# Kernel tuning notes

Hardware: AMD Instinct MI355X
Metric: run time of the kernel (lower is better)

Reference implementation:

```python
import jax, jax.numpy as jnp
import numpy as np

N_NODES = 50000
N_EDGES = 500000
H = 128          # h_dim
HEADS = 3
B = 512          # histories with non-zero length
L = 10           # seq_len (all histories full length)
N_RELS = 200
NEG_SLOPE = 0.2  # DGL GATConv default negative_slope


def setup_inputs() -> dict:
    key = jax.random.key(0)
    ks = jax.random.split(key, 18)
    p = lambda i, shape: jax.random.normal(ks[i], shape, jnp.float32) * 0.05
    return {
        "node_feat": jax.random.normal(ks[0], (N_NODES, H), jnp.float32),
        "W1": p(1, (H, HEADS * H)),
        "attn_l1": p(2, (HEADS, H)),
        "attn_r1": p(3, (HEADS, H)),
        "b1": p(4, (HEADS * H,)),
        "W2": p(5, (H, HEADS * H)),
        "attn_l2": p(6, (HEADS, H)),
        "attn_r2": p(7, (HEADS, H)),
        "b2": p(8, (HEADS * H,)),
        "ent_embeds": jax.random.normal(ks[9], (N_NODES, H), jnp.float32),
        "rel_embeds": jax.random.normal(ks[10], (N_RELS, H), jnp.float32),
        "global_emb_list": jax.random.normal(ks[11], (B * L, H), jnp.float32),
        "s_hist_t": jax.random.uniform(ks[12], (B, L), jnp.float32),
        "edge_src": jax.random.randint(ks[13], (N_EDGES,), 0, N_NODES),
        "edge_dst": jax.random.randint(ks[14], (N_EDGES,), 0, N_NODES),
        "node_ids_graph": jax.random.randint(ks[15], (B * L,), 0, N_NODES),
        "s_tem": jax.random.randint(ks[16], (B,), 0, N_NODES),
        "r_tem": jax.random.randint(ks[17], (B,), 0, N_RELS),
    }


def gat_conv(x, W, attn_l, attn_r, bias, src, dst):
    """DGL-style GATConv (allow_zero_in_degree=True, eval mode)."""
    n = x.shape[0]
    feat = (x @ W).reshape(n, HEADS, H)                    # [N, heads, H]
    el = jnp.einsum('nhd,hd->nh', feat, attn_l)            # [N, heads]
    er = jnp.einsum('nhd,hd->nh', feat, attn_r)
    e = jax.nn.leaky_relu(el[src] + er[dst], NEG_SLOPE)    # [E, heads]
    # edge softmax over incoming edges of each dst node
    emax = jax.ops.segment_max(e, dst, num_segments=n)
    ex = jnp.exp(e - emax[dst])
    denom = jax.ops.segment_sum(ex, dst, num_segments=n)
    alpha = ex / denom[dst]                                # [E, heads]
    msg = alpha[:, :, None] * feat[src]                    # [E, heads, H]
    rst = jax.ops.segment_sum(msg, dst, num_segments=n)    # [N, heads, H]
    return rst + bias.reshape(1, HEADS, H)


def reference(node_feat, W1, attn_l1, attn_r1, b1, W2, attn_l2, attn_r2, b2,
              ent_embeds, rel_embeds, global_emb_list, s_hist_t,
              edge_src, edge_dst, node_ids_graph, s_tem, r_tem):
    h = gat_conv(node_feat, W1, attn_l1, attn_r1, b1, edge_src, edge_dst).mean(axis=1)
    h = gat_conv(h, W2, attn_l2, attn_r2, b2, edge_src, edge_dst).mean(axis=1)
    embeds = h[node_ids_graph].reshape(B, L, H)            # gathered history node embeds
    ent = jnp.broadcast_to(ent_embeds[s_tem][:, None, :], (B, L, H))
    rel = jnp.broadcast_to(rel_embeds[r_tem][:, None, :], (B, L, H))
    glob = global_emb_list.reshape(B, L, H)
    seq = jnp.concatenate([embeds, ent, rel, glob], axis=-1)   # [B, L, 4H]
    seq_r = jnp.concatenate([embeds, ent, glob], axis=-1)      # [B, L, 3H]
    return seq, seq_r, s_hist_t
```

## Files before the change

kernel.cpp:

```cpp
#include <hip/hip_runtime.h>
#include <hip/hip_bf16.h>

#define N_NODES 50000
#define N_EDGES 500000
#define HDIM 128
#define HEADS 3
#define BB 512
#define LL 10
#define NEG_SLOPE 0.2f

typedef __hip_bfloat16 bf16;
typedef unsigned char fp8t;
typedef __bf16 v8bf __attribute__((ext_vector_type(8)));
typedef float f32x4 __attribute__((ext_vector_type(4)));


__global__ void k_zero2(int* a, int na, int* b, int nb){
  int i = blockIdx.x*256 + threadIdx.x;
  if(i < na) a[i] = 0;
  if(i < nb) b[i] = 0;
}

__global__ void k_hist(const int* __restrict__ dst, int* __restrict__ cnt, int E){
  int e = blockIdx.x*256 + threadIdx.x;
  if(e < E) atomicAdd(&cnt[dst[e]], 1);
}


#define SCAN_TILE 2048
#define SCAN_NB ((N_NODES + SCAN_TILE - 1)/SCAN_TILE)

__global__ __launch_bounds__(256) void k_scan_part(const int* __restrict__ cnt,
                                                   int* __restrict__ bsum){
  int b = blockIdx.x, tid = threadIdx.x;
  int i0 = b*SCAN_TILE + tid*8;
  int s = 0;
  #pragma unroll
  for(int j = 0; j < 8; ++j){ int i = i0 + j; s += (i < N_NODES) ? cnt[i] : 0; }
  for(int m = 32; m; m >>= 1) s += __shfl_xor(s, m);
  __shared__ int ws[4];
  if((tid & 63) == 0) ws[tid >> 6] = s;
  __syncthreads();
  if(tid == 0) bsum[b] = ws[0] + ws[1] + ws[2] + ws[3];
}

__global__ __launch_bounds__(64) void k_scan_top(int* __restrict__ bsum, int nb){
  int tid = threadIdx.x;
  int v = (tid < nb) ? bsum[tid] : 0;
  for(int s = 1; s < 64; s <<= 1){
    int t = __shfl_up(v, s);
    if(tid >= s) v += t;
  }
  if(tid < nb) bsum[tid] = v;
}

__global__ __launch_bounds__(256) void k_scan_write(int* __restrict__ cnt,
                                                    const int* __restrict__ bsum,
                                                    int* __restrict__ offs){
  int b = blockIdx.x, tid = threadIdx.x;
  int lane = tid & 63, wv = tid >> 6;
  int i0 = b*SCAN_TILE + tid*8;
  int v[8]; int s = 0;
  #pragma unroll
  for(int j = 0; j < 8; ++j){
    int i = i0 + j;
    v[j] = (i < N_NODES) ? cnt[i] : 0;
    s += v[j];
  }
  #pragma unroll
  for(int j = 0; j < 8; ++j){ int i = i0 + j; if(i < N_NODES) cnt[i] = 0; }
  int incl = s;
  for(int sh = 1; sh < 64; sh <<= 1){
    int t = __shfl_up(incl, sh);
    if(lane >= sh) incl += t;
  }
  __shared__ int wtot[4];
  if(lane == 63) wtot[wv] = incl;
  __syncthreads();
  int woff = 0;
  for(int w = 0; w < wv; ++w) woff += wtot[w];
  int excl = woff + incl - s;
  int run = ((b > 0) ? bsum[b-1] : 0) + excl;
  #pragma unroll
  for(int j = 0; j < 8; ++j){
    int i = i0 + j;
    run += v[j];
    if(i < N_NODES) offs[i+1] = run;
  }
  if(b == 0 && tid == 0) offs[0] = 0;
}

__global__ void k_scatter(const int* __restrict__ src, const int* __restrict__ dst,
                          const int* __restrict__ offs, int* __restrict__ cur,
                          int* __restrict__ csr, int E){
  int e = blockIdx.x*256 + threadIdx.x;
  if(e < E){
    int d = dst[e];
    int p = offs[d] + atomicAdd(&cur[d], 1);
    if(p >= 0 && p < E) csr[p] = src[e];
  }
}


__global__ __launch_bounds__(64) void k_mark(const int* __restrict__ nid,
                                             const int* __restrict__ offs,
                                             const int* __restrict__ csr,
                                             unsigned char* __restrict__ mark){
  unsigned n = (unsigned)nid[blockIdx.x];
  if(n >= N_NODES) return;
  if(threadIdx.x == 0) mark[n] = 1;
  int o0 = offs[n], o1 = offs[n+1];
  for(int j = o0 + (int)threadIdx.x; j < o1; j += 64){
    unsigned s = (unsigned)csr[j];
    if(s < N_NODES) mark[s] = 1;
  }
}


__global__ void k_wt(const float* __restrict__ W, bf16* __restrict__ Wt){
  int i = blockIdx.x*256 + threadIdx.x;
  if(i < HEADS*HDIM*HDIM){
    int n = i >> 7, k = i & 127;
    Wt[i] = __float2bfloat16(W[k*(HEADS*HDIM) + n]);
  }
}


template<int AF32>
__global__ __launch_bounds__(256) void k_gemm(const void* __restrict__ Av,
                                              const bf16* __restrict__ Wt,
                                              const float* __restrict__ al,
                                              const float* __restrict__ ar,
                                              fp8t* __restrict__ feat8,
                                              float* __restrict__ el4,
                                              float* __restrict__ er4, int M){
  int tid  = threadIdx.x;
  int wave = tid >> 6, lane = tid & 63;
  int wr = wave >> 1, wc = wave & 1;
  int row0 = blockIdx.x*64 + wr*32;
  int col0 = blockIdx.y*128 + wc*64;
  int l15 = lane & 15, lhi = lane >> 4;

  f32x4 acc[2][4] = {};
  for(int kk = 0; kk < 4; ++kk){
    int kb = kk*32 + lhi*8;
    v8bf a[2], b[4];
    for(int mi = 0; mi < 2; ++mi){
      int r = row0 + mi*16 + l15;
      if(r >= M) r = M - 1;
      if constexpr(AF32){
        const float* ap = (const float*)Av + (size_t)r*HDIM + kb;
        f32x4 lo = *reinterpret_cast<const f32x4*>(ap);
        f32x4 hi = *reinterpret_cast<const f32x4*>(ap + 4);
        #pragma unroll
        for(int j = 0; j < 4; ++j){ a[mi][j] = (__bf16)lo[j]; a[mi][4+j] = (__bf16)hi[j]; }
      } else {
        a[mi] = *reinterpret_cast<const v8bf*>((const bf16*)Av + (size_t)r*HDIM + kb);
      }
    }
    for(int ni = 0; ni < 4; ++ni){
      int c = col0 + ni*16 + l15;
      b[ni] = *reinterpret_cast<const v8bf*>(Wt + (size_t)c*HDIM + kb);
    }
    for(int mi = 0; mi < 2; ++mi)
      for(int ni = 0; ni < 4; ++ni)
        acc[mi][ni] = __builtin_amdgcn_mfma_f32_16x16x32_bf16(a[mi], b[ni], acc[mi][ni], 0, 0, 0);
  }

  const float* alh = al + blockIdx.y*HDIM;
  const float* arh = ar + blockIdx.y*HDIM;
  float alv[4], arv[4];
  #pragma unroll
  for(int ni = 0; ni < 4; ++ni){
    int d = wc*64 + ni*16 + l15;
    alv[ni] = alh[d]; arv[ni] = arh[d];
  }
  __shared__ float red[2][64][2];
  __shared__ int4 tile4[512];
  fp8t* tile8 = (fp8t*)tile4;

  #pragma unroll
  for(int mi = 0; mi < 2; ++mi){
    #pragma unroll
    for(int j = 0; j < 4; ++j){
      float pe = 0.f, pr = 0.f;
      #pragma unroll
      for(int ni = 0; ni < 4; ++ni){
        pe += acc[mi][ni][j]*alv[ni];
        pr += acc[mi][ni][j]*arv[ni];
      }
      for(int k = 8; k; k >>= 1){ pe += __shfl_xor(pe, k); pr += __shfl_xor(pr, k); }
      int row_l = wr*32 + mi*16 + lhi*4 + j;
      if(l15 == 0){ red[wc][row_l][0] = pe; red[wc][row_l][1] = pr; }
    }
  }
  #pragma unroll
  for(int mi = 0; mi < 2; ++mi)
    #pragma unroll
    for(int j = 0; j < 4; ++j){
      int row_l = wr*32 + mi*16 + lhi*4 + j;
      #pragma unroll
      for(int ni = 0; ni < 4; ++ni){
        float x = acc[mi][ni][j];
        unsigned bb = (unsigned)__builtin_amdgcn_cvt_pk_fp8_f32(x, x, 0, false) & 0xFFu;
        tile8[row_l*128 + wc*64 + ni*16 + l15] = (fp8t)bb;
      }
    }
  __syncthreads();

  if(tid < 64){
    int r = blockIdx.x*64 + tid;
    if(r < M){
      el4[(size_t)r*4 + blockIdx.y] = red[0][tid][0] + red[1][tid][0];
      er4[(size_t)r*4 + blockIdx.y] = red[0][tid][1] + red[1][tid][1];
    }
  }
  #pragma unroll
  for(int pass = 0; pass < 2; ++pass){
    int off = pass*4096 + tid*16;
    int row_l = off >> 7, col = off & 127;
    int r = blockIdx.x*64 + row_l;
    if(r < M)
      *reinterpret_cast<int4*>(feat8 + (size_t)r*(HEADS*HDIM) + blockIdx.y*HDIM + col) =
          tile4[off >> 4];
  }
}


__device__ __forceinline__ float lrelu(float x){ return x > 0.f ? x : NEG_SLOPE*x; }
__device__ __forceinline__ float cvt8(fp8t b){
  return __builtin_amdgcn_cvt_f32_fp8((int)b, 0);
}

#define AGG_CHUNK 128

template<int USE_LIST, int OUT_F32, int USE_MARK>
__global__ __launch_bounds__(128) void k_agg(const fp8t* __restrict__ feat8,
                                             const float* __restrict__ el4,
                                             const float* __restrict__ er4,
                                             const float* __restrict__ bias,
                                             const int* __restrict__ offs,
                                             const int* __restrict__ csr,
                                             const int* __restrict__ list,
                                             const unsigned char* __restrict__ mark,
                                             void* __restrict__ hout){
  int bid = blockIdx.x;
  int n = USE_LIST ? list[bid] : bid;
  if(USE_MARK){ if(!mark[n]) return; }
  int tid = threadIdx.x, lane = tid & 63, wv = tid >> 6;
  __shared__ float s_m[2][3], s_s[2][3];
  __shared__ float s_alpha[AGG_CHUNK][4];
  __shared__ int   s_src[AGG_CHUNK];
  __shared__ float s_facc[HEADS*HDIM];
  int o0 = offs[n];
  int deg = offs[n+1] - o0;
  if(deg < 0 || deg > N_EDGES) deg = 0;
  float4 erv = *reinterpret_cast<const float4*>(er4 + (size_t)n*4);

  if(deg <= AGG_CHUNK){
    float x0 = -1e30f, x1 = -1e30f, x2 = -1e30f; int s = 0;
    if(tid < deg){
      unsigned su = (unsigned)csr[o0 + tid];
      if(su >= N_NODES) su = 0;
      s = (int)su;
      float4 elv = *reinterpret_cast<const float4*>(el4 + (size_t)s*4);
      x0 = lrelu(elv.x + erv.x);
      x1 = lrelu(elv.y + erv.y);
      x2 = lrelu(elv.z + erv.z);
    }
    float m0 = x0, m1 = x1, m2 = x2;
    for(int k = 32; k; k >>= 1){
      m0 = fmaxf(m0, __shfl_xor(m0, k));
      m1 = fmaxf(m1, __shfl_xor(m1, k));
      m2 = fmaxf(m2, __shfl_xor(m2, k));
    }
    if(lane == 0){ s_m[wv][0] = m0; s_m[wv][1] = m1; s_m[wv][2] = m2; }
    __syncthreads();
    m0 = fmaxf(s_m[0][0], s_m[1][0]);
    m1 = fmaxf(s_m[0][1], s_m[1][1]);
    m2 = fmaxf(s_m[0][2], s_m[1][2]);
    float e0 = (tid < deg) ? __expf(x0 - m0) : 0.f;
    float e1 = (tid < deg) ? __expf(x1 - m1) : 0.f;
    float e2 = (tid < deg) ? __expf(x2 - m2) : 0.f;
    float t0 = e0, t1 = e1, t2 = e2;
    for(int k = 32; k; k >>= 1){
      t0 += __shfl_xor(t0, k); t1 += __shfl_xor(t1, k); t2 += __shfl_xor(t2, k);
    }
    if(lane == 0){ s_s[wv][0] = t0; s_s[wv][1] = t1; s_s[wv][2] = t2; }
    if(tid < deg){
      s_src[tid] = s;
      s_alpha[tid][0] = e0; s_alpha[tid][1] = e1; s_alpha[tid][2] = e2;
    }
    __syncthreads();
    if(tid < 96){
      int head = tid >> 5;
      float S = s_s[0][head] + s_s[1][head];
      float ih = (S > 0.f) ? 1.f/S : 0.f;
      float a0 = 0.f, a1 = 0.f, a2 = 0.f, a3 = 0.f;
      for(int i = 0; i < deg; ++i){
        unsigned u = *reinterpret_cast<const unsigned*>(
            feat8 + (size_t)s_src[i]*(HEADS*HDIM) + tid*4);
        float al = s_alpha[i][head];
        a0 += al*__builtin_amdgcn_cvt_f32_fp8((int)u, 0);
        a1 += al*__builtin_amdgcn_cvt_f32_fp8((int)u, 1);
        a2 += al*__builtin_amdgcn_cvt_f32_fp8((int)u, 2);
        a3 += al*__builtin_amdgcn_cvt_f32_fp8((int)u, 3);
      }
      float4 w; w.x = a0*ih; w.y = a1*ih; w.z = a2*ih; w.w = a3*ih;
      *reinterpret_cast<float4*>(s_facc + tid*4) = w;
    }
    __syncthreads();
    float r = (s_facc[tid] + s_facc[HDIM + tid] + s_facc[2*HDIM + tid]
             + bias[tid] + bias[HDIM + tid] + bias[2*HDIM + tid])*(1.f/3.f);
    if(OUT_F32) ((float*)hout)[(size_t)bid*HDIM + tid] = r;
    else        ((bf16*)hout)[(size_t)bid*HDIM + tid] = __float2bfloat16(r);
    return;
  }

  float M0 = -1e30f, M1 = -1e30f, M2 = -1e30f;
  float S0 = 0.f, S1 = 0.f, S2 = 0.f;
  for(int base = 0; base < deg; base += AGG_CHUNK){
    int cn = min(AGG_CHUNK, deg - base);
    float x0 = -1e30f, x1 = -1e30f, x2 = -1e30f;
    if(tid < cn){
      unsigned su = (unsigned)csr[o0 + base + tid];
      if(su >= N_NODES) su = 0;
      float4 elv = *reinterpret_cast<const float4*>(el4 + (size_t)su*4);
      x0 = lrelu(elv.x + erv.x);
      x1 = lrelu(elv.y + erv.y);
      x2 = lrelu(elv.z + erv.z);
    }
    float m0 = x0, m1 = x1, m2 = x2;
    for(int k = 32; k; k >>= 1){
      m0 = fmaxf(m0, __shfl_xor(m0, k));
      m1 = fmaxf(m1, __shfl_xor(m1, k));
      m2 = fmaxf(m2, __shfl_xor(m2, k));
    }
    if(lane == 0){ s_m[wv][0] = m0; s_m[wv][1] = m1; s_m[wv][2] = m2; }
    __syncthreads();
    float nm0 = fmaxf(M0, fmaxf(s_m[0][0], s_m[1][0]));
    float nm1 = fmaxf(M1, fmaxf(s_m[0][1], s_m[1][1]));
    float nm2 = fmaxf(M2, fmaxf(s_m[0][2], s_m[1][2]));
    float e0 = (tid < cn) ? __expf(x0 - nm0) : 0.f;
    float e1 = (tid < cn) ? __expf(x1 - nm1) : 0.f;
    float e2 = (tid < cn) ? __expf(x2 - nm2) : 0.f;
    float t0 = e0, t1 = e1, t2 = e2;
    for(int k = 32; k; k >>= 1){
      t0 += __shfl_xor(t0, k); t1 += __shfl_xor(t1, k); t2 += __shfl_xor(t2, k);
    }
    if(lane == 0){ s_s[wv][0] = t0; s_s[wv][1] = t1; s_s[wv][2] = t2; }
    __syncthreads();
    S0 = S0*__expf(M0 - nm0) + s_s[0][0] + s_s[1][0];
    S1 = S1*__expf(M1 - nm1) + s_s[0][1] + s_s[1][1];
    S2 = S2*__expf(M2 - nm2) + s_s[0][2] + s_s[1][2];
    M0 = nm0; M1 = nm1; M2 = nm2;
  }
  float i0 = 1.f/S0, i1 = 1.f/S1, i2 = 1.f/S2;

  float a0 = 0.f, a1 = 0.f, a2 = 0.f;
  for(int base = 0; base < deg; base += AGG_CHUNK){
    int cn = min(AGG_CHUNK, deg - base);
    __syncthreads();
    if(tid < cn){
      unsigned su = (unsigned)csr[o0 + base + tid];
      if(su >= N_NODES) su = 0;
      float4 elv = *reinterpret_cast<const float4*>(el4 + (size_t)su*4);
      s_src[tid] = (int)su;
      s_alpha[tid][0] = __expf(lrelu(elv.x + erv.x) - M0)*i0;
      s_alpha[tid][1] = __expf(lrelu(elv.y + erv.y) - M1)*i1;
      s_alpha[tid][2] = __expf(lrelu(elv.z + erv.z) - M2)*i2;
    }
    __syncthreads();
    for(int i = 0; i < cn; ++i){
      const fp8t* fr = feat8 + (size_t)s_src[i]*(HEADS*HDIM);
      a0 += s_alpha[i][0]*cvt8(fr[tid]);
      a1 += s_alpha[i][1]*cvt8(fr[HDIM + tid]);
      a2 += s_alpha[i][2]*cvt8(fr[2*HDIM + tid]);
    }
  }
  float r = (a0 + a1 + a2 + bias[tid] + bias[HDIM+tid] + bias[2*HDIM+tid])*(1.f/3.f);
  if(OUT_F32) ((float*)hout)[(size_t)bid*HDIM + tid] = r;
  else        ((bf16*)hout)[(size_t)bid*HDIM + tid] = __float2bfloat16(r);
}


#define SEQ_SZ   (BB*LL*4*HDIM)
#define SEQR_OFF SEQ_SZ
#define SEQR_SZ  (BB*LL*3*HDIM)
#define SH_OFF   (SEQ_SZ + SEQR_SZ)

__global__ __launch_bounds__(128) void k_assemble(const float* __restrict__ h2s,
                                                  const float* __restrict__ ent_e,
                                                  const float* __restrict__ rel_e,
                                                  const float* __restrict__ glob,
                                                  const float* __restrict__ sht,
                                                  const int* __restrict__ s_tem,
                                                  const int* __restrict__ r_tem,
                                                  float* __restrict__ out){
  int p = blockIdx.x;
  int d = threadIdx.x;
  int b = p / LL;
  float emb = h2s[(size_t)p*HDIM + d];
  float ent = ent_e[(size_t)s_tem[b]*HDIM + d];
  float rel = rel_e[(size_t)r_tem[b]*HDIM + d];
  float gl  = glob[(size_t)p*HDIM + d];
  size_t so = (size_t)p*(4*HDIM);
  out[so + d] = emb; out[so + HDIM + d] = ent;
  out[so + 2*HDIM + d] = rel; out[so + 3*HDIM + d] = gl;
  size_t ro = SEQR_OFF + (size_t)p*(3*HDIM);
  out[ro + d] = emb; out[ro + HDIM + d] = ent; out[ro + 2*HDIM + d] = gl;
  if(d == 0) out[SH_OFF + p] = sht[p];
}


extern "C" void kernel_launch(void* const* d_in, const int* in_sizes, int n_in,
                              void* d_out, int out_size, void* d_ws, size_t ws_size,
                              hipStream_t stream){
  const float* node_feat = (const float*)d_in[0];
  const float* W1        = (const float*)d_in[1];
  const float* attn_l1   = (const float*)d_in[2];
  const float* attn_r1   = (const float*)d_in[3];
  const float* b1        = (const float*)d_in[4];
  const float* W2        = (const float*)d_in[5];
  const float* attn_l2   = (const float*)d_in[6];
  const float* attn_r2   = (const float*)d_in[7];
  const float* b2        = (const float*)d_in[8];
  const float* ent_emb   = (const float*)d_in[9];
  const float* rel_emb   = (const float*)d_in[10];
  const float* glob      = (const float*)d_in[11];
  const float* sht       = (const float*)d_in[12];
  const int*  e_src      = (const int*)d_in[13];
  const int*  e_dst      = (const int*)d_in[14];
  const int*  nid        = (const int*)d_in[15];
  const int*  s_tem      = (const int*)d_in[16];
  const int*  r_tem      = (const int*)d_in[17];
  float* out = (float*)d_out;

  char* ws = (char*)d_ws;
  size_t cur_off = 0;
  auto alloc = [&](size_t bytes)->char*{
    char* r = ws + cur_off;
    cur_off += (bytes + 255) & ~(size_t)255;
    return r;
  };
  fp8t*  feat8 = (fp8t*) alloc((size_t)N_NODES*HEADS*HDIM);
  bf16*  h1    = (bf16*) alloc((size_t)N_NODES*HDIM*2);
  float* h2s   = (float*)alloc((size_t)BB*LL*HDIM*4);
  float* el4   = (float*)alloc((size_t)N_NODES*4*4);
  float* er4   = (float*)alloc((size_t)N_NODES*4*4);
  bf16*  wt1   = (bf16*) alloc((size_t)HEADS*HDIM*HDIM*2);
  bf16*  wt2   = (bf16*) alloc((size_t)HEADS*HDIM*HDIM*2);
  int*   offs  = (int*)  alloc((size_t)(N_NODES+1)*4);
  int*   cnt   = (int*)  alloc((size_t)N_NODES*4);
  int*   bsum  = (int*)  alloc((size_t)SCAN_NB*4);
  unsigned char* mark = (unsigned char*)alloc((size_t)N_NODES);
  int*   csr   = (int*)  alloc((size_t)N_EDGES*4);

  k_zero2<<<(N_NODES+255)/256, 256, 0, stream>>>(cnt, N_NODES,
                                                 (int*)mark, (N_NODES+3)/4);
  k_hist<<<(N_EDGES+255)/256, 256, 0, stream>>>(e_dst, cnt, N_EDGES);
  k_scan_part<<<SCAN_NB, 256, 0, stream>>>(cnt, bsum);
  k_scan_top<<<1, 64, 0, stream>>>(bsum, SCAN_NB);
  k_scan_write<<<SCAN_NB, 256, 0, stream>>>(cnt, bsum, offs);
  k_scatter<<<(N_EDGES+255)/256, 256, 0, stream>>>(e_src, e_dst, offs, cnt, csr, N_EDGES);
  k_mark<<<BB*LL, 64, 0, stream>>>(nid, offs, csr, mark);

  k_wt<<<(HEADS*HDIM*HDIM+255)/256, 256, 0, stream>>>(W1, wt1);
  k_wt<<<(HEADS*HDIM*HDIM+255)/256, 256, 0, stream>>>(W2, wt2);

  dim3 ggrid((N_NODES + 63)/64, HEADS);

  k_gemm<1><<<ggrid, 256, 0, stream>>>((const void*)node_feat, wt1, attn_l1, attn_r1,
                                       feat8, el4, er4, N_NODES);
  k_agg<0,0,1><<<N_NODES, 128, 0, stream>>>(feat8, el4, er4, b1, offs, csr,
                                            nullptr, mark, (void*)h1);

  k_gemm<0><<<ggrid, 256, 0, stream>>>((const void*)h1, wt2, attn_l2, attn_r2,
                                       feat8, el4, er4, N_NODES);
  k_agg<1,1,0><<<BB*LL, 128, 0, stream>>>(feat8, el4, er4, b2, offs, csr,
                                          nid, nullptr, (void*)h2s);

  k_assemble<<<BB*LL, 128, 0, stream>>>(h2s, ent_emb, rel_emb, glob, sht,
                                        s_tem, r_tem, out);
}
```

Baseline: 212.8 us.

## Precompute softmax denominators in a separate pass and fuse assembly into aggregation

Adds a per-node kernel that sums the exponentiated attention logits and stores reciprocal denominators, without subtracting the per-node max. The aggregation kernel then computes normalized alphas directly, removing the in-block max and sum wave reductions and their barriers. The final output-assembly kernel is folded into the second aggregation, which drops the h2s intermediate buffer and one launch. The trade-off is an extra launch per layer, and skipping max subtraction risks exp overflow if logits grow large.

```diff
diff --git a/kernel.cpp b/kernel.cpp
--- a/kernel.cpp
+++ b/kernel.cpp
@@ -228,27 +228,70 @@
 
 
 __device__ __forceinline__ float lrelu(float x){ return x > 0.f ? x : NEG_SLOPE*x; }
-__device__ __forceinline__ float cvt8(fp8t b){
-  return __builtin_amdgcn_cvt_f32_fp8((int)b, 0);
-}
+
+template<int USE_LIST, int USE_MARK>
+__global__ __launch_bounds__(256) void k_denom(const float* __restrict__ el4,
+                                               const float* __restrict__ er4,
+                                               const int* __restrict__ offs,
+                                               const int* __restrict__ csr,
+                                               const int* __restrict__ list,
+                                               const unsigned char* __restrict__ mark,
+                                               float* __restrict__ inv4, int total){
+  int i = blockIdx.x*256 + threadIdx.x;
+  if(i >= total) return;
+  unsigned n = USE_LIST ? (unsigned)list[i] : (unsigned)i;
+  if(n >= N_NODES) return;
+  if(USE_MARK){ if(!mark[n]) return; }
+  int o0 = offs[n];
+  int deg = offs[n+1] - o0;
+  if(deg < 0 || deg > N_EDGES) deg = 0;
+  float4 erv = *reinterpret_cast<const float4*>(er4 + (size_t)n*4);
+  float S0 = 0.f, S1 = 0.f, S2 = 0.f;
+  for(int j = 0; j < deg; ++j){
+    unsigned s = (unsigned)csr[o0 + j];
+    if(s >= N_NODES) s = 0;
+    float4 elv = *reinterpret_cast<const float4*>(el4 + (size_t)s*4);
+    S0 += __expf(lrelu(elv.x + erv.x));
+    S1 += __expf(lrelu(elv.y + erv.y));
+    S2 += __expf(lrelu(elv.z + erv.z));
+  }
+  float4 iv;
+  iv.x = (S0 > 0.f) ? 1.f/S0 : 0.f;
+  iv.y = (S1 > 0.f) ? 1.f/S1 : 0.f;
+  iv.z = (S2 > 0.f) ? 1.f/S2 : 0.f;
+  iv.w = 0.f;
+  *reinterpret_cast<float4*>(inv4 + (size_t)n*4) = iv;
+}
+
 
 #define AGG_CHUNK 128
-
-template<int USE_LIST, int OUT_F32, int USE_MARK>
+#define SEQ_SZ   (BB*LL*4*HDIM)
+#define SEQR_OFF SEQ_SZ
+#define SEQR_SZ  (BB*LL*3*HDIM)
+#define SH_OFF   (SEQ_SZ + SEQR_SZ)
+
+template<int USE_LIST, int FUSED, int USE_MARK>
 __global__ __launch_bounds__(128) void k_agg(const fp8t* __restrict__ feat8,
                                              const float* __restrict__ el4,
                                              const float* __restrict__ er4,
+                                             const float* __restrict__ inv4,
                                              const float* __restrict__ bias,
                                              const int* __restrict__ offs,
                                              const int* __restrict__ csr,
                                              const int* __restrict__ list,
                                              const unsigned char* __restrict__ mark,
-                                             void* __restrict__ hout){
+                                             bf16* __restrict__ h1,
+                                             const float* __restrict__ ent_e,
+                                             const float* __restrict__ rel_e,
+                                             const float* __restrict__ glob,
+                                             const float* __restrict__ sht,
+                                             const int* __restrict__ s_tem,
+                                             const int* __restrict__ r_tem,
+                                             float* __restrict__ out){
   int bid = blockIdx.x;
   int n = USE_LIST ? list[bid] : bid;
   if(USE_MARK){ if(!mark[n]) return; }
-  int tid = threadIdx.x, lane = tid & 63, wv = tid >> 6;
-  __shared__ float s_m[2][3], s_s[2][3];
+  int tid = threadIdx.x;
   __shared__ float s_alpha[AGG_CHUNK][4];
   __shared__ int   s_src[AGG_CHUNK];
   __shared__ float s_facc[HEADS*HDIM];
@@ -256,48 +299,25 @@
   int deg = offs[n+1] - o0;
   if(deg < 0 || deg > N_EDGES) deg = 0;
   float4 erv = *reinterpret_cast<const float4*>(er4 + (size_t)n*4);
-
-  if(deg <= AGG_CHUNK){
-    float x0 = -1e30f, x1 = -1e30f, x2 = -1e30f; int s = 0;
-    if(tid < deg){
-      unsigned su = (unsigned)csr[o0 + tid];
+  float4 iv  = *reinterpret_cast<const float4*>(inv4 + (size_t)n*4);
+
+  float a0 = 0.f, a1 = 0.f, a2 = 0.f, a3 = 0.f;
+  int head = tid >> 5;
+  for(int base = 0; base < deg; base += AGG_CHUNK){
+    int cn = min(AGG_CHUNK, deg - base);
+    if(base) __syncthreads();
+    if(tid < cn){
+      unsigned su = (unsigned)csr[o0 + base + tid];
       if(su >= N_NODES) su = 0;
-      s = (int)su;
-      float4 elv = *reinterpret_cast<const float4*>(el4 + (size_t)s*4);
-      x0 = lrelu(elv.x + erv.x);
-      x1 = lrelu(elv.y + erv.y);
-      x2 = lrelu(elv.z + erv.z);
-    }
-    float m0 = x0, m1 = x1, m2 = x2;
-    for(int k = 32; k; k >>= 1){
-      m0 = fmaxf(m0, __shfl_xor(m0, k));
-      m1 = fmaxf(m1, __shfl_xor(m1, k));
-      m2 = fmaxf(m2, __shfl_xor(m2, k));
-    }
-    if(lane == 0){ s_m[wv][0] = m0; s_m[wv][1] = m1; s_m[wv][2] = m2; }
-    __syncthreads();
-    m0 = fmaxf(s_m[0][0], s_m[1][0]);
-    m1 = fmaxf(s_m[0][1], s_m[1][1]);
-    m2 = fmaxf(s_m[0][2], s_m[1][2]);
-    float e0 = (tid < deg) ? __expf(x0 - m0) : 0.f;
-    float e1 = (tid < deg) ? __expf(x1 - m1) : 0.f;
-    float e2 = (tid < deg) ? __expf(x2 - m2) : 0.f;
-    float t0 = e0, t1 = e1, t2 = e2;
-    for(int k = 32; k; k >>= 1){
-      t0 += __shfl_xor(t0, k); t1 += __shfl_xor(t1, k); t2 += __shfl_xor(t2, k);
-    }
-    if(lane == 0){ s_s[wv][0] = t0; s_s[wv][1] = t1; s_s[wv][2] = t2; }
-    if(tid < deg){
-      s_src[tid] = s;
-      s_alpha[tid][0] = e0; s_alpha[tid][1] = e1; s_alpha[tid][2] = e2;
+      float4 elv = *reinterpret_cast<const float4*>(el4 + (size_t)su*4);
+      s_src[tid] = (int)su;
+      s_alpha[tid][0] = __expf(lrelu(elv.x + erv.x))*iv.x;
+      s_alpha[tid][1] = __expf(lrelu(elv.y + erv.y))*iv.y;
+      s_alpha[tid][2] = __expf(lrelu(elv.z + erv.z))*iv.z;
     }
     __syncthreads();
     if(tid < 96){
-      int head = tid >> 5;
-      float S = s_s[0][head] + s_s[1][head];
-      float ih = (S > 0.f) ? 1.f/S : 0.f;
-      float a0 = 0.f, a1 = 0.f, a2 = 0.f, a3 = 0.f;
-      for(int i = 0; i < deg; ++i){
+      for(int i = 0; i < cn; ++i){
         unsigned u = *reinterpret_cast<const unsigned*>(
             feat8 + (size_t)s_src[i]*(HEADS*HDIM) + tid*4);
         float al = s_alpha[i][head];
@@ -306,110 +326,29 @@
         a2 += al*__builtin_amdgcn_cvt_f32_fp8((int)u, 2);
         a3 += al*__builtin_amdgcn_cvt_f32_fp8((int)u, 3);
       }
-      float4 w; w.x = a0*ih; w.y = a1*ih; w.z = a2*ih; w.w = a3*ih;
-      *reinterpret_cast<float4*>(s_facc + tid*4) = w;
-    }
-    __syncthreads();
-    float r = (s_facc[tid] + s_facc[HDIM + tid] + s_facc[2*HDIM + tid]
-             + bias[tid] + bias[HDIM + tid] + bias[2*HDIM + tid])*(1.f/3.f);
-    if(OUT_F32) ((float*)hout)[(size_t)bid*HDIM + tid] = r;
-    else        ((bf16*)hout)[(size_t)bid*HDIM + tid] = __float2bfloat16(r);
-    return;
-  }
-
-  float M0 = -1e30f, M1 = -1e30f, M2 = -1e30f;
-  float S0 = 0.f, S1 = 0.f, S2 = 0.f;
-  for(int base = 0; base < deg; base += AGG_CHUNK){
-    int cn = min(AGG_CHUNK, deg - base);
-    float x0 = -1e30f, x1 = -1e30f, x2 = -1e30f;
-    if(tid < cn){
-      unsigned su = (unsigned)csr[o0 + base + tid];
-      if(su >= N_NODES) su = 0;
-      float4 elv = *reinterpret_cast<const float4*>(el4 + (size_t)su*4);
-      x0 = lrelu(elv.x + erv.x);
-      x1 = lrelu(elv.y + erv.y);
-      x2 = lrelu(elv.z + erv.z);
-    }
-    float m0 = x0, m1 = x1, m2 = x2;
-    for(int k = 32; k; k >>= 1){
-      m0 = fmaxf(m0, __shfl_xor(m0, k));
-      m1 = fmaxf(m1, __shfl_xor(m1, k));
-      m2 = fmaxf(m2, __shfl_xor(m2, k));
-    }
-    if(lane == 0){ s_m[wv][0] = m0; s_m[wv][1] = m1; s_m[wv][2] = m2; }
-    __syncthreads();
-    float nm0 = fmaxf(M0, fmaxf(s_m[0][0], s_m[1][0]));
-    float nm1 = fmaxf(M1, fmaxf(s_m[0][1], s_m[1][1]));
-    float nm2 = fmaxf(M2, fmaxf(s_m[0][2], s_m[1][2]));
-    float e0 = (tid < cn) ? __expf(x0 - nm0) : 0.f;
-    float e1 = (tid < cn) ? __expf(x1 - nm1) : 0.f;
-    float e2 = (tid < cn) ? __expf(x2 - nm2) : 0.f;
-    float t0 = e0, t1 = e1, t2 = e2;
-    for(int k = 32; k; k >>= 1){
-      t0 += __shfl_xor(t0, k); t1 += __shfl_xor(t1, k); t2 += __shfl_xor(t2, k);
-    }
-    if(lane == 0){ s_s[wv][0] = t0; s_s[wv][1] = t1; s_s[wv][2] = t2; }
-    __syncthreads();
-    S0 = S0*__expf(M0 - nm0) + s_s[0][0] + s_s[1][0];
-    S1 = S1*__expf(M1 - nm1) + s_s[0][1] + s_s[1][1];
-    S2 = S2*__expf(M2 - nm2) + s_s[0][2] + s_s[1][2];
-    M0 = nm0; M1 = nm1; M2 = nm2;
-  }
-  float i0 = 1.f/S0, i1 = 1.f/S1, i2 = 1.f/S2;
-
-  float a0 = 0.f, a1 = 0.f, a2 = 0.f;
-  for(int base = 0; base < deg; base += AGG_CHUNK){
-    int cn = min(AGG_CHUNK, deg - base);
-    __syncthreads();
-    if(tid < cn){
-      unsigned su = (unsigned)csr[o0 + base + tid];
-      if(su >= N_NODES) su = 0;
-      float4 elv = *reinterpret_cast<const float4*>(el4 + (size_t)su*4);
-      s_src[tid] = (int)su;
-      s_alpha[tid][0] = __expf(lrelu(elv.x + erv.x) - M0)*i0;
-      s_alpha[tid][1] = __expf(lrelu(elv.y + erv.y) - M1)*i1;
-      s_alpha[tid][2] = __expf(lrelu(elv.z + erv.z) - M2)*i2;
-    }
-    __syncthreads();
-    for(int i = 0; i < cn; ++i){
-      const fp8t* fr = feat8 + (size_t)s_src[i]*(HEADS*HDIM);
-      a0 += s_alpha[i][0]*cvt8(fr[tid]);
-      a1 += s_alpha[i][1]*cvt8(fr[HDIM + tid]);
-      a2 += s_alpha[i][2]*cvt8(fr[2*HDIM + tid]);
-    }
-  }
-  float r = (a0 + a1 + a2 + bias[tid] + bias[HDIM+tid] + bias[2*HDIM+tid])*(1.f/3.f);
-  if(OUT_F32) ((float*)hout)[(size_t)bid*HDIM + tid] = r;
-  else        ((bf16*)hout)[(size_t)bid*HDIM + tid] = __float2bfloat16(r);
-}
-
-
-#define SEQ_SZ   (BB*LL*4*HDIM)
-#define SEQR_OFF SEQ_SZ
-#define SEQR_SZ  (BB*LL*3*HDIM)
-#define SH_OFF   (SEQ_SZ + SEQR_SZ)
-
-__global__ __launch_bounds__(128) void k_assemble(const float* __restrict__ h2s,
-                                                  const float* __restrict__ ent_e,
-                                                  const float* __restrict__ rel_e,
-                                                  const float* __restrict__ glob,
-                                                  const float* __restrict__ sht,
-                                                  const int* __restrict__ s_tem,
-                                                  const int* __restrict__ r_tem,
-                                                  float* __restrict__ out){
-  int p = blockIdx.x;
-  int d = threadIdx.x;
-  int b = p / LL;
-  float emb = h2s[(size_t)p*HDIM + d];
-  float ent = ent_e[(size_t)s_tem[b]*HDIM + d];
-  float rel = rel_e[(size_t)r_tem[b]*HDIM + d];
-  float gl  = glob[(size_t)p*HDIM + d];
-  size_t so = (size_t)p*(4*HDIM);
-  out[so + d] = emb; out[so + HDIM + d] = ent;
-  out[so + 2*HDIM + d] = rel; out[so + 3*HDIM + d] = gl;
-  size_t ro = SEQR_OFF + (size_t)p*(3*HDIM);
-  out[ro + d] = emb; out[ro + HDIM + d] = ent; out[ro + 2*HDIM + d] = gl;
-  if(d == 0) out[SH_OFF + p] = sht[p];
+    }
+  }
+  if(tid < 96){
+    float4 w; w.x = a0; w.y = a1; w.z = a2; w.w = a3;
+    *reinterpret_cast<float4*>(s_facc + tid*4) = w;
+  }
+  __syncthreads();
+  float r = (s_facc[tid] + s_facc[HDIM + tid] + s_facc[2*HDIM + tid]
+           + bias[tid] + bias[HDIM + tid] + bias[2*HDIM + tid])*(1.f/3.f);
+  if(FUSED){
+    int p = bid, b = p/LL, d = tid;
+    float ent = ent_e[(size_t)s_tem[b]*HDIM + d];
+    float rel = rel_e[(size_t)r_tem[b]*HDIM + d];
+    float gl  = glob[(size_t)p*HDIM + d];
+    size_t so = (size_t)p*(4*HDIM);
+    out[so + d] = r; out[so + HDIM + d] = ent;
+    out[so + 2*HDIM + d] = rel; out[so + 3*HDIM + d] = gl;
+    size_t ro = SEQR_OFF + (size_t)p*(3*HDIM);
+    out[ro + d] = r; out[ro + HDIM + d] = ent; out[ro + 2*HDIM + d] = gl;
+    if(d == 0) out[SH_OFF + p] = sht[p];
+  } else {
+    h1[(size_t)n*HDIM + tid] = __float2bfloat16(r);
+  }
 }
 
 
@@ -445,9 +384,9 @@
   };
   fp8t*  feat8 = (fp8t*) alloc((size_t)N_NODES*HEADS*HDIM);
   bf16*  h1    = (bf16*) alloc((size_t)N_NODES*HDIM*2);
-  float* h2s   = (float*)alloc((size_t)BB*LL*HDIM*4);
   float* el4   = (float*)alloc((size_t)N_NODES*4*4);
   float* er4   = (float*)alloc((size_t)N_NODES*4*4);
+  float* inv4  = (float*)alloc((size_t)N_NODES*4*4);
   bf16*  wt1   = (bf16*) alloc((size_t)HEADS*HDIM*HDIM*2);
   bf16*  wt2   = (bf16*) alloc((size_t)HEADS*HDIM*HDIM*2);
   int*   offs  = (int*)  alloc((size_t)(N_NODES+1)*4);
@@ -472,14 +411,19 @@
 
   k_gemm<1><<<ggrid, 256, 0, stream>>>((const void*)node_feat, wt1, attn_l1, attn_r1,
                                        feat8, el4, er4, N_NODES);
-  k_agg<0,0,1><<<N_NODES, 128, 0, stream>>>(feat8, el4, er4, b1, offs, csr,
-                                            nullptr, mark, (void*)h1);
+  k_denom<0,1><<<(N_NODES+255)/256, 256, 0, stream>>>(el4, er4, offs, csr,
+                                                      nullptr, mark, inv4, N_NODES);
+  k_agg<0,0,1><<<N_NODES, 128, 0, stream>>>(feat8, el4, er4, inv4, b1, offs, csr,
+                                            nullptr, mark, h1,
+                                            nullptr, nullptr, nullptr, nullptr,
+                                            nullptr, nullptr, nullptr);
 
   k_gemm<0><<<ggrid, 256, 0, stream>>>((const void*)h1, wt2, attn_l2, attn_r2,
                                        feat8, el4, er4, N_NODES);
-  k_agg<1,1,0><<<BB*LL, 128, 0, stream>>>(feat8, el4, er4, b2, offs, csr,
-                                          nid, nullptr, (void*)h2s);
-
-  k_assemble<<<BB*LL, 128, 0, stream>>>(h2s, ent_emb, rel_emb, glob, sht,
-                                        s_tem, r_tem, out);
-}
+  k_denom<1,0><<<(BB*LL+255)/256, 256, 0, stream>>>(el4, er4, offs, csr,
+                                                    nid, nullptr, inv4, BB*LL);
+  k_agg<1,1,0><<<BB*LL, 128, 0, stream>>>(feat8, el4, er4, inv4, b2, offs, csr,
+                                          nid, nullptr, nullptr,
+                                          ent_emb, rel_emb, glob, sht,
+                                          s_tem, r_tem, out);
+}
```

Measured after the change: 225.5 us. 6.0% more time.
